# Performance work log

Measured on AMD Instinct MI355X. Metric: run time of the kernel, lower is better.

## Reference

```python
import jax, jax.numpy as jnp
import numpy as np
from jax import ops as jops

N_NODES = 100000
N_EDGES = 1600000
NEG_SLOPE = 0.2
LN_EPS = 1e-5


def setup_inputs() -> dict:
    key = jax.random.key(0)
    ks = jax.random.split(key, 12)
    inp = {
        "x": jax.random.normal(ks[0], (N_NODES, 4), jnp.float32),
        "edge_index": jax.random.randint(ks[1], (2, N_EDGES), 0, N_NODES, jnp.int64 if jax.config.jax_enable_x64 else jnp.int32),
        # layer 1: GATv2Conv(4, 16, heads=4)
        "W1l": jax.random.normal(ks[2], (4, 64), jnp.float32) * 0.5,
        "W1r": jax.random.normal(ks[3], (4, 64), jnp.float32) * 0.5,
        "a1": jax.random.normal(ks[4], (4, 16), jnp.float32) * 0.5,  # [heads, out]
        "b1": jax.random.normal(ks[5], (64,), jnp.float32) * 0.1,
        "g1": jnp.ones((64,), jnp.float32),
        "be1": jnp.zeros((64,), jnp.float32),
        # layer 2: GATv2Conv(64, 32, heads=1)
        "W2l": jax.random.normal(ks[6], (64, 32), jnp.float32) * 0.125,
        "W2r": jax.random.normal(ks[7], (64, 32), jnp.float32) * 0.125,
        "a2": jax.random.normal(ks[8], (1, 32), jnp.float32) * 0.5,
        "b2": jax.random.normal(ks[9], (32,), jnp.float32) * 0.1,
        "g2": jnp.ones((32,), jnp.float32),
        "be2": jnp.zeros((32,), jnp.float32),
    }
    return inp


def _add_self_loops(edge_index, n):
    loop = jnp.arange(n, dtype=edge_index.dtype)
    return jnp.concatenate([edge_index, jnp.stack([loop, loop])], axis=1)


def _gatv2(x, src, dst, Wl, Wr, att, bias, heads, out_ch, n):
    # x: [N, F]; Wl/Wr: [F, heads*out_ch]; att: [heads, out_ch]
    xl = (x @ Wl).reshape(n, heads, out_ch)  # source transform
    xr = (x @ Wr).reshape(n, heads, out_ch)  # target transform
    e = xl[src] + xr[dst]                     # [E, H, C]
    e = jnp.where(e >= 0, e, NEG_SLOPE * e)   # LeakyReLU(0.2)
    logits = jnp.einsum('ehc,hc->eh', e, att)  # [E, H]
    # segment softmax over destination node
    m = jops.segment_max(logits, dst, num_segments=n)  # [N, H]
    ex = jnp.exp(logits - m[dst])
    denom = jops.segment_sum(ex, dst, num_segments=n)  # [N, H]
    alpha = ex / denom[dst]                            # [E, H]
    out = jops.segment_sum(alpha[:, :, None] * xl[src], dst, num_segments=n)  # [N, H, C]
    return out.reshape(n, heads * out_ch) + bias


def _layernorm(x, g, b):
    mu = jnp.mean(x, axis=-1, keepdims=True)
    var = jnp.mean(jnp.square(x - mu), axis=-1, keepdims=True)
    return (x - mu) * jax.lax.rsqrt(var + LN_EPS) * g + b


def reference(x, edge_index, W1l, W1r, a1, b1, g1, be1, W2l, W2r, a2, b2, g2, be2):
    n = x.shape[0]
    ei = _add_self_loops(edge_index, n)
    src, dst = ei[0], ei[1]
    h = _gatv2(x, src, dst, W1l, W1r, a1, b1, heads=4, out_ch=16, n=n)
    h = _layernorm(h, g1, be1)
    h = jnp.where(h > 0, h, jnp.expm1(h))  # ELU
    h = _gatv2(h, src, dst, W2l, W2r, a2, b2, heads=1, out_ch=32, n=n)
    h = _layernorm(h, g2, be2)
    return h
```

## Files before the change

### kernel.cpp

```cpp
#include <hip/hip_runtime.h>
#include <math.h>

#define NN 100000
#define E0 1600000
#define ETOT (E0 + NN)
#define NEG 0.2f

#define NB 512
#define BS 196
#define CHUNK 4096
#define PPT 16
#define MAXP 4096

template <int CTRL>
__device__ __forceinline__ float dppadd(float v) {
    int t = __builtin_amdgcn_update_dpp(0, __float_as_int(v), CTRL, 0xf, 0xf, true);
    return v + __int_as_float(t);
}
__device__ __forceinline__ float wsum64(float v) {
    v = dppadd<0xB1>(v);
    v = dppadd<0x4E>(v);
    v = dppadd<0x141>(v);
    v = dppadd<0x140>(v);
    v += __shfl_xor(v, 16);
    v += __shfl_xor(v, 32);
    return v;
}
__device__ __forceinline__ unsigned f2bf_rn(float f) {
    unsigned u = __float_as_uint(f);
    return (u + 0x7FFFu + ((u >> 16) & 1u)) >> 16;
}

__global__ void k_bhist(const int* __restrict__ ei, int* __restrict__ bcnt) {
    __shared__ int h[NB];
    int tid = threadIdx.x;
    for (int i = tid; i < NB; i += 256) h[i] = 0;
    __syncthreads();
    int stride = gridDim.x * 256;
    for (int e = blockIdx.x * 256 + tid; e < E0; e += stride)
        atomicAdd(&h[ei[E0 + e] / BS], 1);
    __syncthreads();
    for (int i = tid; i < NB; i += 256)
        if (h[i]) atomicAdd(&bcnt[i], h[i]);
}

__global__ void k_bscan(const int* __restrict__ bcnt, int* __restrict__ boff,
                        int* __restrict__ srcsBase, int* __restrict__ cursor,
                        int* __restrict__ rs) {
    __shared__ int s[NB];
    int tid = threadIdx.x;
    int v = bcnt[tid];
    s[tid] = v;
    __syncthreads();
    for (int off = 1; off < NB; off <<= 1) {
        int t = (tid >= off) ? s[tid - off] : 0;
        __syncthreads();
        s[tid] += t;
        __syncthreads();
    }
    int excl = s[tid] - v;
    boff[tid] = excl;
    cursor[tid] = excl;
    int n0 = tid * BS;
    if (n0 > NN) n0 = NN;
    srcsBase[tid] = excl + n0;
    if (tid == 0) rs[NN] = ETOT;
}

__global__ void k_bin(const int* __restrict__ ei, int* __restrict__ cursor,
                      int2* __restrict__ binned) {
    __shared__ int hist[NB];
    __shared__ int basesh[NB];
    int tid = threadIdx.x;
    long long cbase = (long long)blockIdx.x * CHUNK;
    for (int i = tid; i < NB; i += 256) hist[i] = 0;
    __syncthreads();
    int srcv[PPT], dstv[PPT], rank[PPT], bkt[PPT];
#pragma unroll
    for (int k = 0; k < PPT; ++k) {
        long long e = cbase + k * 256 + tid;
        if (e < E0) {
            int s_ = ei[e];
            int d_ = ei[E0 + e];
            int b = d_ / BS;
            rank[k] = atomicAdd(&hist[b], 1);
            srcv[k] = s_;
            dstv[k] = d_;
            bkt[k] = b;
        } else {
            bkt[k] = -1;
        }
    }
    __syncthreads();
    for (int i = tid; i < NB; i += 256)
        if (hist[i] > 0) basesh[i] = atomicAdd(&cursor[i], hist[i]);
    __syncthreads();
#pragma unroll
    for (int k = 0; k < PPT; ++k)
        if (bkt[k] >= 0) {
            int2 p;
            p.x = srcv[k];
            p.y = dstv[k];
            binned[basesh[bkt[k]] + rank[k]] = p;
        }
}

__global__ void k_bfin(const int2* __restrict__ binned, const int* __restrict__ bcnt,
                       const int* __restrict__ boff, const int* __restrict__ srcsBase,
                       int* __restrict__ rs, int* __restrict__ srcs) {
    int b = blockIdx.x;
    int n0 = b * BS;
    if (n0 >= NN) return;
    int nd = NN - n0;
    if (nd > BS) nd = BS;
    int cnt = bcnt[b];
    if (cnt > MAXP) cnt = MAXP;
    int base = boff[b];
    int sb = srcsBase[b];
    __shared__ int ldsCnt[256];
    __shared__ int scanA[256];
    __shared__ int rowOffE[256];
    __shared__ int stage[MAXP + BS];
    int tid = threadIdx.x;
    ldsCnt[tid] = 0;
    __syncthreads();
    int srcv[PPT], dl_[PPT], rk_[PPT];
#pragma unroll
    for (int k = 0; k < PPT; ++k) {
        int i = k * 256 + tid;
        if (i < cnt) {
            int2 p = binned[base + i];
            int dl = p.y - n0;
            rk_[k] = atomicAdd(&ldsCnt[dl], 1);
            srcv[k] = p.x;
            dl_[k] = dl;
        } else {
            dl_[k] = -1;
        }
    }
    __syncthreads();
    int v = (tid < nd) ? ldsCnt[tid] + 1 : 0;
    scanA[tid] = v;
    __syncthreads();
    for (int off = 1; off < 256; off <<= 1) {
        int t = (tid >= off) ? scanA[tid - off] : 0;
        __syncthreads();
        scanA[tid] += t;
        __syncthreads();
    }
    rowOffE[tid] = scanA[tid] - v;
    __syncthreads();
    if (tid < nd) {
        int e = rowOffE[tid];
        rs[n0 + tid] = sb + e;
        stage[e] = n0 + tid;
    }
    __syncthreads();
#pragma unroll
    for (int k = 0; k < PPT; ++k)
        if (dl_[k] >= 0) stage[rowOffE[dl_[k]] + 1 + rk_[k]] = srcv[k];
    __syncthreads();
    int tot = cnt + nd;
    for (int i = tid; i < tot; i += 256) srcs[sb + i] = stage[i];
}

__global__ void k_gat1(const float* __restrict__ x, const float* __restrict__ Wl,
                       const float* __restrict__ Wr, const float* __restrict__ att,
                       const int* __restrict__ rs, const int* __restrict__ srcs,
                       const float* __restrict__ b, const float* __restrict__ g,
                       const float* __restrict__ be, float* __restrict__ h) {
    int lane = threadIdx.x & 63;
    int wave = (blockIdx.x * blockDim.x + threadIdx.x) >> 6;
    int nwaves = (gridDim.x * blockDim.x) >> 6;
    int e_i = lane >> 3;
    int sub = lane & 7;
    float wl[4][8], wr[4][8], at[8];
#pragma unroll
    for (int k = 0; k < 4; ++k)
#pragma unroll
        for (int j = 0; j < 8; ++j) {
            wl[k][j] = Wl[k * 64 + sub * 8 + j];
            wr[k][j] = Wr[k * 64 + sub * 8 + j];
        }
#pragma unroll
    for (int j = 0; j < 8; ++j) at[j] = att[sub * 8 + j];

    for (int n = wave; n < NN; n += nwaves) {
        const float4 xd = *(const float4*)(x + (long long)n * 4);
        float xrd[8];
#pragma unroll
        for (int j = 0; j < 8; ++j)
            xrd[j] = xd.x * wr[0][j] + xd.y * wr[1][j] + xd.z * wr[2][j] +
                     xd.w * wr[3][j];
        int beg = rs[n];
        int end = rs[n + 1];
        float acc4[4] = {0.f, 0.f, 0.f, 0.f};
        float den = 0.f;
        int slot = beg + e_i;
        bool valid = slot < end;
        int s = srcs[valid ? slot : beg];
        float4 xa = *(const float4*)(x + (long long)s * 4);
        for (int base = beg; base < end; base += 8) {
            int nslot = base + 8 + e_i;
            bool nvalid = nslot < end;
            int ns = srcs[nvalid ? nslot : beg];
            float4 xn = *(const float4*)(x + (long long)ns * 4);
            float p = 0.f;
#pragma unroll
            for (int j = 0; j < 8; ++j) {
                float t = xa.x * wl[0][j] + xa.y * wl[1][j] + xa.z * wl[2][j] +
                          xa.w * wl[3][j];
                float u = t + xrd[j];
                u = fmaxf(u, NEG * u);
                p += u * at[j];
            }
            p = dppadd<0xB1>(p);
            float ex = valid ? __expf(p) : 0.f;
            den += ex;
            acc4[0] += ex * xa.x;
            acc4[1] += ex * xa.y;
            acc4[2] += ex * xa.z;
            acc4[3] += ex * xa.w;
            xa = xn;
            valid = nvalid;
        }
#pragma unroll
        for (int m = 8; m <= 32; m <<= 1) {
#pragma unroll
            for (int k = 0; k < 4; ++k) acc4[k] += __shfl_xor(acc4[k], m);
            den += __shfl_xor(den, m);
        }
        int cf = sub * 8 + e_i;
        float v = (acc4[0] * Wl[cf] + acc4[1] * Wl[64 + cf] +
                   acc4[2] * Wl[128 + cf] + acc4[3] * Wl[192 + cf]) / den + b[cf];
        float mu = wsum64(v) * (1.f / 64.f);
        float c = v - mu;
        float var = wsum64(c * c) * (1.f / 64.f);
        float y = c * rsqrtf(var + 1e-5f) * g[cf] + be[cf];
        h[(long long)n * 64 + cf] = y > 0.f ? y : expm1f(y);
    }
}

__global__ void k_lin2(const float* __restrict__ h, const float* __restrict__ Wl,
                       const float* __restrict__ Wr, unsigned* __restrict__ xl2p,
                       float* __restrict__ xr2) {
    __shared__ float wl_s[2048];
    __shared__ float wr_s[2048];
    for (int i = threadIdx.x; i < 2048; i += blockDim.x) {
        wl_s[i] = Wl[i];
        wr_s[i] = Wr[i];
    }
    __syncthreads();
    int t = blockIdx.x * blockDim.x + threadIdx.x;
    if (t >= NN * 16) return;
    int n = t >> 4, j2 = t & 15;
    const float* hr = h + (long long)n * 64;
    float al0 = 0.f, al1 = 0.f, ar0 = 0.f, ar1 = 0.f;
#pragma unroll 8
    for (int k = 0; k < 64; ++k) {
        float hv = hr[k];
        al0 += hv * wl_s[k * 32 + j2 * 2];
        al1 += hv * wl_s[k * 32 + j2 * 2 + 1];
        ar0 += hv * wr_s[k * 32 + j2 * 2];
        ar1 += hv * wr_s[k * 32 + j2 * 2 + 1];
    }
    xl2p[(long long)n * 16 + j2] = (f2bf_rn(al1) << 16) | f2bf_rn(al0);
    *(float2*)(xr2 + (long long)n * 32 + j2 * 2) = {ar0, ar1};
}

__global__ void k_gat2(const unsigned* __restrict__ xl2p,
                       const float* __restrict__ xr2,
                       const float* __restrict__ att, const int* __restrict__ rs,
                       const int* __restrict__ srcs, const float* __restrict__ b,
                       const float* __restrict__ g, const float* __restrict__ be,
                       float* __restrict__ out) {
    int lane = threadIdx.x & 63;
    int wave = (blockIdx.x * blockDim.x + threadIdx.x) >> 6;
    int nwaves = (gridDim.x * blockDim.x) >> 6;
    int e_i = lane >> 3;
    int cg = lane & 7;
    float at[4];
#pragma unroll
    for (int j = 0; j < 4; ++j) at[j] = att[cg * 4 + j];

    for (int n = wave; n < NN; n += nwaves) {
        const float4 xr4 = *(const float4*)(xr2 + (long long)n * 32 + cg * 4);
        float xrd[4] = {xr4.x, xr4.y, xr4.z, xr4.w};
        int beg = rs[n];
        int end = rs[n + 1];
        float acc[4] = {0.f, 0.f, 0.f, 0.f};
        float den = 0.f;
        int slot = beg + e_i;
        bool valid = slot < end;
        int s = srcs[valid ? slot : beg];
        uint2 xp = *(const uint2*)(xl2p + (long long)s * 16 + cg * 2);
        for (int base = beg; base < end; base += 8) {
            int nslot = base + 8 + e_i;
            bool nvalid = nslot < end;
            int ns = srcs[nvalid ? nslot : beg];
            uint2 xq = *(const uint2*)(xl2p + (long long)ns * 16 + cg * 2);
            float xv0 = __uint_as_float(xp.x << 16);
            float xv1 = __uint_as_float(xp.x & 0xFFFF0000u);
            float xv2 = __uint_as_float(xp.y << 16);
            float xv3 = __uint_as_float(xp.y & 0xFFFF0000u);
            float u0 = xv0 + xrd[0], u1 = xv1 + xrd[1];
            float u2 = xv2 + xrd[2], u3 = xv3 + xrd[3];
            u0 = fmaxf(u0, NEG * u0);
            u1 = fmaxf(u1, NEG * u1);
            u2 = fmaxf(u2, NEG * u2);
            u3 = fmaxf(u3, NEG * u3);
            float p = u0 * at[0] + u1 * at[1] + u2 * at[2] + u3 * at[3];
            p = dppadd<0xB1>(p);
            p = dppadd<0x4E>(p);
            p = dppadd<0x141>(p);
            float ex = valid ? __expf(p) : 0.f;
            den += ex;
            acc[0] += ex * xv0;
            acc[1] += ex * xv1;
            acc[2] += ex * xv2;
            acc[3] += ex * xv3;
            xp = xq;
            valid = nvalid;
        }
#pragma unroll
        for (int m = 8; m <= 32; m <<= 1) {
#pragma unroll
            for (int j = 0; j < 4; ++j) acc[j] += __shfl_xor(acc[j], m);
            den += __shfl_xor(den, m);
        }
        int e3 = e_i & 3;
        float v = acc[0];
#pragma unroll
        for (int j = 1; j < 4; ++j) v = (e3 == j) ? acc[j] : v;
        int cf = cg * 4 + e3;
        v = v / den + b[cf];
        float mu = wsum64(v) * (1.f / 64.f);
        float cc = v - mu;
        float var = wsum64(cc * cc) * (1.f / 64.f);
        float y = cc * rsqrtf(var + 1e-5f) * g[cf] + be[cf];
        if (e_i < 4) out[(long long)n * 32 + cf] = y;
    }
}

extern "C" void kernel_launch(void* const* d_in, const int* in_sizes, int n_in,
                              void* d_out, int out_size, void* d_ws, size_t ws_size,
                              hipStream_t stream) {
    const float* x   = (const float*)d_in[0];
    const int*   ei  = (const int*)d_in[1];
    const float* W1l = (const float*)d_in[2];
    const float* W1r = (const float*)d_in[3];
    const float* a1  = (const float*)d_in[4];
    const float* b1  = (const float*)d_in[5];
    const float* g1  = (const float*)d_in[6];
    const float* be1 = (const float*)d_in[7];
    const float* W2l = (const float*)d_in[8];
    const float* W2r = (const float*)d_in[9];
    const float* a2  = (const float*)d_in[10];
    const float* b2  = (const float*)d_in[11];
    const float* g2  = (const float*)d_in[12];
    const float* be2 = (const float*)d_in[13];
    float* out = (float*)d_out;

    float* ws = (float*)d_ws;
    float* h   = ws;
    unsigned* xl2p = (unsigned*)(ws + 6400000);
    float* xr2 = ws + 9600000;
    int2* binned = (int2*)ws;
    int* ib        = (int*)(ws + 12800000);
    int* rs        = ib;
    int* srcs      = ib + 100001;
    int* bcnt      = ib + 1800100;
    int* boff      = ib + 1800100 + NB;
    int* srcsBase  = ib + 1800100 + 2 * NB;
    int* cursor    = ib + 1800100 + 3 * NB;

    hipMemsetAsync(bcnt, 0, NB * sizeof(int), stream);
    k_bhist<<<256, 256, 0, stream>>>(ei, bcnt);
    k_bscan<<<1, NB, 0, stream>>>(bcnt, boff, srcsBase, cursor, rs);
    k_bin<<<(E0 + CHUNK - 1) / CHUNK, 256, 0, stream>>>(ei, cursor, binned);
    k_bfin<<<NB, 256, 0, stream>>>(binned, bcnt, boff, srcsBase, rs, srcs);

    k_gat1<<<2048, 256, 0, stream>>>(x, W1l, W1r, a1, rs, srcs, b1, g1, be1, h);
    k_lin2<<<(NN * 16 + 255) / 256, 256, 0, stream>>>(h, W2l, W2r, xl2p, xr2);
    k_gat2<<<2048, 256, 0, stream>>>(xl2p, xr2, a2, rs, srcs, b2, g2, be2, out);
}
```

Measured before the change: 218.8 us.

## Precompute layer-1 target transform and remap gat1 lanes to 16 features x 4 edges

Adds a kernel that precomputes x@W1r into a 64-wide buffer, so gat1 loads it instead of recomputing it per node. gat1 is reorganised so each lane handles 4 features over 4 edges per iteration rather than 8 features over 8 edges. The software prefetch of the next edge is dropped, and LayerNorm now uses a single-pass sum/sum-of-squares variance. The aim is fewer registers per lane and fewer FLOPs per edge, at the cost of an extra kernel launch and 25.6MB of extra memory traffic, plus twice as many loop iterations per node.

```diff
diff --git a/kernel.cpp b/kernel.cpp
--- a/kernel.cpp
+++ b/kernel.cpp
@@ -164,79 +164,87 @@
     for (int i = tid; i < tot; i += 256) srcs[sb + i] = stage[i];
 }
 
+__global__ void k_linr(const float* __restrict__ x, const float* __restrict__ Wr,
+                       float* __restrict__ xr1) {
+    int t = blockIdx.x * blockDim.x + threadIdx.x;
+    if (t >= NN * 16) return;
+    int n = t >> 4;
+    int j = (t & 15) << 2;
+    const float4 xv = *(const float4*)(x + (long long)n * 4);
+    float4 a = {0.f, 0.f, 0.f, 0.f};
+#pragma unroll
+    for (int k = 0; k < 4; ++k) {
+        float4 w = *(const float4*)(Wr + k * 64 + j);
+        float xk = k == 0 ? xv.x : k == 1 ? xv.y : k == 2 ? xv.z : xv.w;
+        a.x += xk * w.x; a.y += xk * w.y;
+        a.z += xk * w.z; a.w += xk * w.w;
+    }
+    *(float4*)(xr1 + (long long)n * 64 + j) = a;
+}
+
 __global__ void k_gat1(const float* __restrict__ x, const float* __restrict__ Wl,
-                       const float* __restrict__ Wr, const float* __restrict__ att,
+                       const float* __restrict__ xr1, const float* __restrict__ att,
                        const int* __restrict__ rs, const int* __restrict__ srcs,
                        const float* __restrict__ b, const float* __restrict__ g,
                        const float* __restrict__ be, float* __restrict__ h) {
     int lane = threadIdx.x & 63;
     int wave = (blockIdx.x * blockDim.x + threadIdx.x) >> 6;
     int nwaves = (gridDim.x * blockDim.x) >> 6;
-    int e_i = lane >> 3;
-    int sub = lane & 7;
-    float wl[4][8], wr[4][8], at[8];
+    int sub = lane & 15;
+    int e_i = lane >> 4;
+    float wl[4][4], at4[4];
 #pragma unroll
     for (int k = 0; k < 4; ++k)
 #pragma unroll
-        for (int j = 0; j < 8; ++j) {
-            wl[k][j] = Wl[k * 64 + sub * 8 + j];
-            wr[k][j] = Wr[k * 64 + sub * 8 + j];
-        }
-#pragma unroll
-    for (int j = 0; j < 8; ++j) at[j] = att[sub * 8 + j];
+        for (int j = 0; j < 4; ++j) wl[k][j] = Wl[k * 64 + sub * 4 + j];
+#pragma unroll
+    for (int j = 0; j < 4; ++j) at4[j] = att[sub * 4 + j];
 
     for (int n = wave; n < NN; n += nwaves) {
-        const float4 xd = *(const float4*)(x + (long long)n * 4);
-        float xrd[8];
-#pragma unroll
-        for (int j = 0; j < 8; ++j)
-            xrd[j] = xd.x * wr[0][j] + xd.y * wr[1][j] + xd.z * wr[2][j] +
-                     xd.w * wr[3][j];
+        const float4 xr = *(const float4*)(xr1 + (long long)n * 64 + sub * 4);
+        float xrd[4] = {xr.x, xr.y, xr.z, xr.w};
         int beg = rs[n];
         int end = rs[n + 1];
-        float acc4[4] = {0.f, 0.f, 0.f, 0.f};
-        float den = 0.f;
-        int slot = beg + e_i;
-        bool valid = slot < end;
-        int s = srcs[valid ? slot : beg];
-        float4 xa = *(const float4*)(x + (long long)s * 4);
-        for (int base = beg; base < end; base += 8) {
-            int nslot = base + 8 + e_i;
-            bool nvalid = nslot < end;
-            int ns = srcs[nvalid ? nslot : beg];
-            float4 xn = *(const float4*)(x + (long long)ns * 4);
+        float a0 = 0.f, a1 = 0.f, a2 = 0.f, a3 = 0.f, den = 0.f;
+        for (int base = beg; base < end; base += 4) {
+            int slot = base + e_i;
+            bool valid = slot < end;
+            int s = srcs[valid ? slot : beg];
+            const float4 xa = *(const float4*)(x + (long long)s * 4);
             float p = 0.f;
 #pragma unroll
-            for (int j = 0; j < 8; ++j) {
+            for (int j = 0; j < 4; ++j) {
                 float t = xa.x * wl[0][j] + xa.y * wl[1][j] + xa.z * wl[2][j] +
                           xa.w * wl[3][j];
                 float u = t + xrd[j];
                 u = fmaxf(u, NEG * u);
-                p += u * at[j];
+                p += u * at4[j];
             }
             p = dppadd<0xB1>(p);
+            p = dppadd<0x4E>(p);
             float ex = valid ? __expf(p) : 0.f;
             den += ex;
-            acc4[0] += ex * xa.x;
-            acc4[1] += ex * xa.y;
-            acc4[2] += ex * xa.z;
-            acc4[3] += ex * xa.w;
-            xa = xn;
-            valid = nvalid;
-        }
-#pragma unroll
-        for (int m = 8; m <= 32; m <<= 1) {
-#pragma unroll
-            for (int k = 0; k < 4; ++k) acc4[k] += __shfl_xor(acc4[k], m);
+            a0 += ex * xa.x;
+            a1 += ex * xa.y;
+            a2 += ex * xa.z;
+            a3 += ex * xa.w;
+        }
+#pragma unroll
+        for (int m = 16; m <= 32; m <<= 1) {
+            a0 += __shfl_xor(a0, m);
+            a1 += __shfl_xor(a1, m);
+            a2 += __shfl_xor(a2, m);
+            a3 += __shfl_xor(a3, m);
             den += __shfl_xor(den, m);
         }
-        int cf = sub * 8 + e_i;
-        float v = (acc4[0] * Wl[cf] + acc4[1] * Wl[64 + cf] +
-                   acc4[2] * Wl[128 + cf] + acc4[3] * Wl[192 + cf]) / den + b[cf];
-        float mu = wsum64(v) * (1.f / 64.f);
-        float c = v - mu;
-        float var = wsum64(c * c) * (1.f / 64.f);
-        float y = c * rsqrtf(var + 1e-5f) * g[cf] + be[cf];
+        int cf = (sub >> 2) * 16 + (sub & 3) * 4 + e_i;
+        float v = (a0 * Wl[cf] + a1 * Wl[64 + cf] + a2 * Wl[128 + cf] +
+                   a3 * Wl[192 + cf]) / den + b[cf];
+        float s1 = wsum64(v);
+        float s2 = wsum64(v * v);
+        float mu = s1 * (1.f / 64.f);
+        float var = fmaxf(s2 * (1.f / 64.f) - mu * mu, 0.f);
+        float y = (v - mu) * rsqrtf(var + 1e-5f) * g[cf] + be[cf];
         h[(long long)n * 64 + cf] = y > 0.f ? y : expm1f(y);
     }
 }
@@ -363,6 +371,7 @@
 
     float* ws = (float*)d_ws;
     float* h   = ws;
+    float* xr1 = ws + 6400000;
     unsigned* xl2p = (unsigned*)(ws + 6400000);
     float* xr2 = ws + 9600000;
     int2* binned = (int2*)ws;
@@ -379,8 +388,9 @@
     k_bscan<<<1, NB, 0, stream>>>(bcnt, boff, srcsBase, cursor, rs);
     k_bin<<<(E0 + CHUNK - 1) / CHUNK, 256, 0, stream>>>(ei, cursor, binned);
     k_bfin<<<NB, 256, 0, stream>>>(binned, bcnt, boff, srcsBase, rs, srcs);
-
-    k_gat1<<<2048, 256, 0, stream>>>(x, W1l, W1r, a1, rs, srcs, b1, g1, be1, h);
+    k_linr<<<(NN * 16 + 255) / 256, 256, 0, stream>>>(x, W1r, xr1);
+
+    k_gat1<<<2048, 256, 0, stream>>>(x, W1l, xr1, a1, rs, srcs, b1, g1, be1, h);
     k_lin2<<<(NN * 16 + 255) / 256, 256, 0, stream>>>(h, W2l, W2r, xl2p, xr2);
     k_gat2<<<2048, 256, 0, stream>>>(xl2p, xr2, a2, rs, srcs, b2, g2, be2, out);
 }
```

Result: slower. 234.3 us (+7.1%).
